# Kernel optimization log

Measured on AMD Instinct MI355X. Metric: run time of the kernel, lower is better.

The kernel has to match this reference:

```python
import math
import jax, jax.numpy as jnp
import numpy as np

B, S, D, H = 2, 2048, 1024, 16
DH = D // H
DFF = 4 * D
EPS = 1e-6
MASKED_BIAS = -10000.0


def _gelu(x):
    # GPT-2 tanh-approx GELU
    return 0.5 * x * (1.0 + jnp.tanh(math.sqrt(2.0 / math.pi) * (x + 0.044715 * x ** 3)))


def _layernorm(x, w, b):
    mean = jnp.mean(x, axis=-1, keepdims=True)
    var = jnp.mean((x - mean) ** 2, axis=-1, keepdims=True)
    return w * ((x - mean) / jnp.sqrt(var + EPS)) + b


def setup_inputs() -> dict:
    key = jax.random.key(0)
    ks = jax.random.split(key, 6)
    std = 0.02
    return {
        "hidden_states": jax.random.normal(ks[0], (B, S, D), jnp.float32),
        "w_attn": jax.random.normal(ks[1], (D, 3 * D), jnp.float32) * std,
        "b_attn": jnp.zeros((3 * D,), jnp.float32),
        "w_proj": jax.random.normal(ks[2], (D, D), jnp.float32) * std,
        "b_proj": jnp.zeros((D,), jnp.float32),
        "w_fc": jax.random.normal(ks[3], (D, DFF), jnp.float32) * std,
        "b_fc": jnp.zeros((DFF,), jnp.float32),
        "w_fc_proj": jax.random.normal(ks[4], (DFF, D), jnp.float32) * std,
        "b_fc_proj": jnp.zeros((D,), jnp.float32),
        "ln1_w": jnp.ones((D,), jnp.float32),
        "ln1_b": jnp.zeros((D,), jnp.float32),
        "ln2_w": jnp.ones((D,), jnp.float32),
        "ln2_b": jnp.zeros((D,), jnp.float32),
    }


def reference(hidden_states, w_attn, b_attn, w_proj, b_proj, w_fc, b_fc,
              w_fc_proj, b_fc_proj, ln1_w, ln1_b, ln2_w, ln2_b):
    residual = hidden_states
    x = _layernorm(hidden_states, ln1_w, ln1_b)

    # c_attn: [B,S,D] @ [D,3D] + b -> split into q,k,v
    qkv = x @ w_attn + b_attn
    q, k, v = jnp.split(qkv, 3, axis=-1)
    # split heads -> [B,H,S,DH]
    q = q.reshape(B, S, H, DH).transpose(0, 2, 1, 3)
    k = k.reshape(B, S, H, DH).transpose(0, 2, 1, 3)
    v = v.reshape(B, S, H, DH).transpose(0, 2, 1, 3)

    scores = jnp.einsum('bhqd,bhkd->bhqk', q, k) / jnp.sqrt(jnp.float32(DH))
    causal = jnp.tril(jnp.ones((S, S), bool))  # [S,S]
    scores = jnp.where(causal[None, None], scores, jnp.float32(MASKED_BIAS))
    attn = jax.nn.softmax(scores, axis=-1)
    out = jnp.einsum('bhqk,bhkd->bhqd', attn, v)
    out = out.transpose(0, 2, 1, 3).reshape(B, S, D)
    out = out @ w_proj + b_proj

    h = residual + out
    residual = h
    y = _layernorm(h, ln2_w, ln2_b)
    y = _gelu(y @ w_fc + b_fc)
    y = y @ w_fc_proj + b_fc_proj
    return residual + y
```

## Files before the change

kernel.cpp:

```cpp
#include <hip/hip_runtime.h>
#include <cstdint>
#include <cstddef>

typedef unsigned short u16;
typedef float  floatx4 __attribute__((ext_vector_type(4)));
typedef short  short8  __attribute__((ext_vector_type(8)));
typedef u16    usx4    __attribute__((ext_vector_type(4)));
typedef u16    usx8    __attribute__((ext_vector_type(8)));
typedef unsigned uintx2 __attribute__((ext_vector_type(2)));

__device__ __forceinline__ u16 f2b(float f) {
  unsigned u = __float_as_uint(f);
  unsigned r = u + 0x7fffu + ((u >> 16) & 1u);
  return (u16)(r >> 16);
}
__device__ __forceinline__ float b2f(u16 s) {
  return __uint_as_float(((unsigned)s) << 16);
}

__device__ __forceinline__ unsigned cvt_pk_bf16(float lo, float hi) {
  unsigned r;
  asm("v_cvt_pk_bf16_f32 %0, %1, %2" : "=v"(r) : "v"(lo), "v"(hi));
  return r;
}

__device__ __forceinline__ float rowmax16(float x) {
  int xi = __float_as_int(x), y;
  y = __builtin_amdgcn_update_dpp(xi, xi, 0xB1, 0xF, 0xF, false);
  x = fmaxf(x, __int_as_float(y)); xi = __float_as_int(x);
  y = __builtin_amdgcn_update_dpp(xi, xi, 0x4E, 0xF, 0xF, false);
  x = fmaxf(x, __int_as_float(y)); xi = __float_as_int(x);
  y = __builtin_amdgcn_update_dpp(xi, xi, 0x141, 0xF, 0xF, false);
  x = fmaxf(x, __int_as_float(y)); xi = __float_as_int(x);
  y = __builtin_amdgcn_update_dpp(xi, xi, 0x140, 0xF, 0xF, false);
  x = fmaxf(x, __int_as_float(y));
  return x;
}

__device__ __forceinline__ float gelu_f(float x) {
  const float k = 2.3022082f;
  float u = x * (1.0f + 0.044715f * x * x);
  float t = __builtin_amdgcn_exp2f(-k * u);
  return x * __builtin_amdgcn_rcpf(1.0f + t);
}

__device__ __forceinline__ void gl2lds16(const u16* g, u16* l) {
  __builtin_amdgcn_global_load_lds(
      (const __attribute__((address_space(1))) unsigned int*)g,
      (__attribute__((address_space(3))) unsigned int*)l, 16, 0, 0);
}

template<int N> __device__ __forceinline__ void wait_stage_barrier() {
  asm volatile("s_waitcnt vmcnt(%0)" :: "n"(N) : "memory");
  __builtin_amdgcn_s_barrier();
  __builtin_amdgcn_sched_barrier(0);
}

#define C2SCALE 0.18033688011112042f

__global__ __launch_bounds__(256) void ln_bf16_kernel(
    const float* __restrict__ in, const float* __restrict__ w,
    const float* __restrict__ b, u16* __restrict__ out)
{
  const int row = blockIdx.x;
  const int t = threadIdx.x;
  const float* p = in + (size_t)row * 1024 + t * 4;
  floatx4 v = *(const floatx4*)p;
  float s  = v.x + v.y + v.z + v.w;
  float ss = v.x*v.x + v.y*v.y + v.z*v.z + v.w*v.w;
  #pragma unroll
  for (int m = 1; m < 64; m <<= 1) {
    s  += __shfl_xor(s,  m);
    ss += __shfl_xor(ss, m);
  }
  __shared__ float red[8];
  if ((t & 63) == 0) { red[(t >> 6)*2] = s; red[(t >> 6)*2 + 1] = ss; }
  __syncthreads();
  s  = red[0] + red[2] + red[4] + red[6];
  ss = red[1] + red[3] + red[5] + red[7];
  const float mean = s * (1.0f / 1024.0f);
  const float var  = ss * (1.0f / 1024.0f) - mean * mean;
  const float rstd = rsqrtf(var + 1e-6f);
  floatx4 wv = *(const floatx4*)(w + t * 4);
  floatx4 bv = *(const floatx4*)(b + t * 4);
  usx4 o = { f2b(wv.x * ((v.x - mean) * rstd) + bv.x),
             f2b(wv.y * ((v.y - mean) * rstd) + bv.y),
             f2b(wv.z * ((v.z - mean) * rstd) + bv.z),
             f2b(wv.w * ((v.w - mean) * rstd) + bv.w) };
  *(usx4*)(out + (size_t)row * 1024 + t * 4) = o;
}

template<int NP>
__global__ __launch_bounds__(256) void combine_ln_kernel(
    const u16* __restrict__ pp, size_t pstride,
    const float* __restrict__ res, const float* __restrict__ bias,
    const float* __restrict__ w, const float* __restrict__ b,
    float* __restrict__ hout, u16* __restrict__ yout)
{
  const int row = blockIdx.x;
  const int t = threadIdx.x;
  const size_t i0 = (size_t)row * 1024 + t * 4;
  floatx4 rv = *(const floatx4*)(res + i0);
  usx4 a[NP];
  #pragma unroll
  for (int z = 0; z < NP; ++z) a[z] = *(const usx4*)(pp + z * pstride + i0);
  floatx4 biasv = *(const floatx4*)(bias + t * 4);
  floatx4 v;
  #pragma unroll
  for (int i = 0; i < 4; ++i) {
    float acc = rv[i] + biasv[i];
    #pragma unroll
    for (int z = 0; z < NP; ++z) acc += b2f(a[z][i]);
    v[i] = acc;
  }
  *(floatx4*)(hout + i0) = v;

  float s  = v.x + v.y + v.z + v.w;
  float ss = v.x*v.x + v.y*v.y + v.z*v.z + v.w*v.w;
  #pragma unroll
  for (int m = 1; m < 64; m <<= 1) {
    s  += __shfl_xor(s,  m);
    ss += __shfl_xor(ss, m);
  }
  __shared__ float red[8];
  if ((t & 63) == 0) { red[(t >> 6)*2] = s; red[(t >> 6)*2 + 1] = ss; }
  __syncthreads();
  s  = red[0] + red[2] + red[4] + red[6];
  ss = red[1] + red[3] + red[5] + red[7];
  const float mean = s * (1.0f / 1024.0f);
  const float var  = ss * (1.0f / 1024.0f) - mean * mean;
  const float rstd = rsqrtf(var + 1e-6f);
  floatx4 wv = *(const floatx4*)(w + t * 4);
  floatx4 bv = *(const floatx4*)(b + t * 4);
  usx4 o = { f2b(wv.x * ((v.x - mean) * rstd) + bv.x),
             f2b(wv.y * ((v.y - mean) * rstd) + bv.y),
             f2b(wv.z * ((v.z - mean) * rstd) + bv.z),
             f2b(wv.w * ((v.w - mean) * rstd) + bv.w) };
  *(usx4*)(yout + i0) = o;
}

__device__ __forceinline__ void wtrans_body(
    const float* __restrict__ in, u16* __restrict__ out, int K, int N,
    int bx, int by, int tx, int ty)
{
  __shared__ u16 tile[32][33];
  const int n0 = bx * 32, k0 = by * 32;
  #pragma unroll
  for (int i = 0; i < 4; ++i)
    tile[ty + i*8][tx] = f2b(in[(size_t)(k0 + ty + i*8) * N + n0 + tx]);
  __syncthreads();
  #pragma unroll
  for (int i = 0; i < 4; ++i)
    out[(size_t)(n0 + ty + i*8) * K + k0 + tx] = tile[tx][ty + i*8];
}

__global__ __launch_bounds__(256) void wtrans4_kernel(
    const float* __restrict__ w0, const float* __restrict__ w1,
    const float* __restrict__ w2, const float* __restrict__ w3,
    u16* __restrict__ o0, u16* __restrict__ o1,
    u16* __restrict__ o2, u16* __restrict__ o3)
{
  int blk = blockIdx.x;
  const int tx = threadIdx.x & 31, ty = threadIdx.x >> 5;
  if (blk < 3072) {
    wtrans_body(w0, o0, 1024, 3072, blk % 96, blk / 96, tx, ty);
  } else if (blk < 4096) {
    blk -= 3072; wtrans_body(w1, o1, 1024, 1024, blk % 32, blk / 32, tx, ty);
  } else if (blk < 8192) {
    blk -= 4096; wtrans_body(w2, o2, 1024, 4096, blk % 128, blk / 128, tx, ty);
  } else {
    blk -= 8192; wtrans_body(w3, o3, 4096, 1024, blk % 32, blk / 32, tx, ty);
  }
}

template<int FLAGS, int NX, int NY, int NZ, int RX, int RY, int RZ>
__global__ __launch_bounds__(512, 2) void gemm256_kernel(
    const u16* __restrict__ A, const u16* __restrict__ Bt,
    const float* __restrict__ bias,
    void* __restrict__ Cout, int M, int N, int K, int kLen, size_t zStride)
{
  constexpr int SLOT = 256 * 32;
  constexpr int GX = NX / RX, GY = NY / RY, GZ = NZ / RZ;
  __shared__ u16 As[2][2][SLOT];
  __shared__ u16 Bs[2][2][SLOT];

  const int lin = blockIdx.x + NX * (blockIdx.y + NY * blockIdx.z);
  const int xcd = lin & 7;
  const int idx = lin >> 3;
  const int rx = xcd % RX, ry = (xcd / RX) % RY, rz = xcd / (RX * RY);
  const int bx = rx * GX + idx % GX;
  const int by = ry * GY + (idx / GX) % GY;
  const int bz = rz * GZ + idx / (GX * GY);

  const int t = threadIdx.x;
  const int wave = t >> 6;
  const int lane = t & 63;
  const int quad = lane >> 4, l16 = lane & 15;
  const int wm = wave >> 2;
  const int wn = wave & 3;
  const int bm0 = by * 256, bn0 = bx * 256;
  const int kStart = bz * kLen;

  const int sRow = lane >> 2;
  const int sq   = (lane & 3) ^ ((lane >> 3) & 3);

  const u16* aGb[2]; const u16* bGb[2];
  #pragma unroll
  for (int j = 0; j < 2; ++j) {
    const int band = wave * 2 + j;
    aGb[j] = A  + (size_t)(bm0 + band * 16 + sRow) * K + kStart + sq * 8;
    bGb[j] = Bt + (size_t)(bn0 + band * 16 + sRow) * K + kStart + sq * 8;
  }

  auto stageA = [&](int kt, int kk) {
    u16* dst = &As[kt & 1][kk][0];
    #pragma unroll
    for (int j = 0; j < 2; ++j)
      gl2lds16(aGb[j] + kt * 64 + kk * 32, dst + (wave * 2 + j) * 512);
  };
  auto stageB = [&](int kt, int kk) {
    u16* dst = &Bs[kt & 1][kk][0];
    #pragma unroll
    for (int j = 0; j < 2; ++j)
      gl2lds16(bGb[j] + kt * 64 + kk * 32, dst + (wave * 2 + j) * 512);
  };

  floatx4 acc[8][4] = {};
  const int rcol = (quad ^ ((l16 >> 1) & 3)) << 3;

  const int NT = kLen >> 6;
  stageA(0, 0); stageB(0, 0); stageA(0, 1); stageB(0, 1);

  #pragma unroll 1
  for (int kt = 0; kt < NT; ++kt) {
    const int buf = kt & 1;
    const bool pf = (kt + 1 < NT);
    short8 af[4], bf[4];

    wait_stage_barrier<4>();
    #pragma unroll
    for (int nt2 = 0; nt2 < 4; ++nt2)
      bf[nt2] = *(const short8*)&Bs[buf][0][(wn*64 + nt2*16 + l16) * 32 + rcol];
    #pragma unroll
    for (int mt = 0; mt < 4; ++mt)
      af[mt] = *(const short8*)&As[buf][0][(wm*128 + mt*16 + l16) * 32 + rcol];
    if (pf) stageA(kt + 1, 0);
    __builtin_amdgcn_s_barrier();
    asm volatile("s_waitcnt lgkmcnt(0)" ::: "memory");
    __builtin_amdgcn_sched_barrier(0);
    __builtin_amdgcn_s_setprio(1);
    #pragma unroll
    for (int mt = 0; mt < 4; ++mt)
      #pragma unroll
      for (int nt2 = 0; nt2 < 4; ++nt2)
        acc[mt][nt2] = __builtin_amdgcn_mfma_f32_16x16x32_bf16(af[mt], bf[nt2], acc[mt][nt2], 0, 0, 0);
    __builtin_amdgcn_s_setprio(0);
    __builtin_amdgcn_s_barrier();
    #pragma unroll
    for (int mt = 0; mt < 4; ++mt)
      af[mt] = *(const short8*)&As[buf][0][(wm*128 + (mt+4)*16 + l16) * 32 + rcol];
    if (pf) stageB(kt + 1, 0);
    __builtin_amdgcn_s_barrier();
    asm volatile("s_waitcnt lgkmcnt(0)" ::: "memory");
    __builtin_amdgcn_sched_barrier(0);
    __builtin_amdgcn_s_setprio(1);
    #pragma unroll
    for (int mt = 0; mt < 4; ++mt)
      #pragma unroll
      for (int nt2 = 0; nt2 < 4; ++nt2)
        acc[mt+4][nt2] = __builtin_amdgcn_mfma_f32_16x16x32_bf16(af[mt], bf[nt2], acc[mt+4][nt2], 0, 0, 0);
    __builtin_amdgcn_s_setprio(0);
    if (pf) wait_stage_barrier<4>(); else wait_stage_barrier<0>();
    #pragma unroll
    for (int nt2 = 0; nt2 < 4; ++nt2)
      bf[nt2] = *(const short8*)&Bs[buf][1][(wn*64 + nt2*16 + l16) * 32 + rcol];
    #pragma unroll
    for (int mt = 0; mt < 4; ++mt)
      af[mt] = *(const short8*)&As[buf][1][(wm*128 + mt*16 + l16) * 32 + rcol];
    if (pf) stageA(kt + 1, 1);
    __builtin_amdgcn_s_barrier();
    asm volatile("s_waitcnt lgkmcnt(0)" ::: "memory");
    __builtin_amdgcn_sched_barrier(0);
    __builtin_amdgcn_s_setprio(1);
    #pragma unroll
    for (int mt = 0; mt < 4; ++mt)
      #pragma unroll
      for (int nt2 = 0; nt2 < 4; ++nt2)
        acc[mt][nt2] = __builtin_amdgcn_mfma_f32_16x16x32_bf16(af[mt], bf[nt2], acc[mt][nt2], 0, 0, 0);
    __builtin_amdgcn_s_setprio(0);
    __builtin_amdgcn_s_barrier();
    #pragma unroll
    for (int mt = 0; mt < 4; ++mt)
      af[mt] = *(const short8*)&As[buf][1][(wm*128 + (mt+4)*16 + l16) * 32 + rcol];
    if (pf) stageB(kt + 1, 1);
    __builtin_amdgcn_s_barrier();
    asm volatile("s_waitcnt lgkmcnt(0)" ::: "memory");
    __builtin_amdgcn_sched_barrier(0);
    __builtin_amdgcn_s_setprio(1);
    #pragma unroll
    for (int mt = 0; mt < 4; ++mt)
      #pragma unroll
      for (int nt2 = 0; nt2 < 4; ++nt2)
        acc[mt+4][nt2] = __builtin_amdgcn_mfma_f32_16x16x32_bf16(af[mt], bf[nt2], acc[mt+4][nt2], 0, 0, 0);
    __builtin_amdgcn_s_setprio(0);
  }

  const int orow0 = bm0 + wm * 128;
  const int ocol0 = bn0 + wn * 64;
  const size_t zoff = (size_t)bz * zStride;
  #pragma unroll
  for (int nt2 = 0; nt2 < 4; ++nt2) {
    const int col = ocol0 + nt2*16 + l16;
    const float bv = bias ? bias[col] : 0.0f;
    const float postscale = ((FLAGS & 8) && col < 1024) ? C2SCALE : 1.0f;
    #pragma unroll
    for (int mt = 0; mt < 8; ++mt) {
      #pragma unroll
      for (int r = 0; r < 4; ++r) {
        const int row = orow0 + mt*16 + quad*4 + r;
        float v = acc[mt][nt2][r] + bv;
        if (FLAGS & 1) v = gelu_f(v);
        if (FLAGS & 8) v *= postscale;
        if (FLAGS & 4) ((u16*)Cout)[zoff + (size_t)row * N + col] = f2b(v);
        else           ((float*)Cout)[zoff + (size_t)row * N + col] = v;
      }
    }
  }
}

__global__ __launch_bounds__(256, 4) void attn_mfma_kernel(
    const u16* __restrict__ qkv, u16* __restrict__ opart, float* __restrict__ ml)
{
  __shared__ u16 Ks[64][72];
  __shared__ u16 Vt[64][72];
  __shared__ u16 Ps[64][72];

  const int t    = threadIdx.x;
  const int wave = t >> 6;
  const int lane = t & 63;
  const int quad = lane >> 4;
  const int l16  = lane & 15;
  const int pair = blockIdx.x >> 1;
  const int half = blockIdx.x & 1;
  const int h    = blockIdx.y;
  const int b    = blockIdx.z;

  const size_t base = (size_t)b * 2048 * 3072;
  const int qoff = h * 64;
  const int koff = 1024 + h * 64;
  const int voff = 2048 + h * 64;

  const int prow = t >> 2;
  const int scol = (t & 3) * 16;
  const int kmap = ((prow & 15) << 2) | (prow >> 4);
  const int kpair  = t & 31;
  const int vchunk = t >> 5;

  const size_t obase  = ((((size_t)half * 2 + b) * 16 + h) * 2048) * 64;
  const size_t mlbase = ((((size_t)half * 2 + b) * 16 + h) * 2048) * 2;

  short8 onesb;
  {
    const short v = (l16 == 0) ? (short)0x3F80 : (short)0;
    #pragma unroll
    for (int i = 0; i < 8; ++i) onesb[i] = v;
  }

  #pragma unroll 1
  for (int iter = 0; iter < 2; ++iter) {
    const int qi = iter ? (31 - pair) : pair;
    const int q0 = qi << 6;
    const int T  = qi + 1;
    const int mid = (T + 1) >> 1;
    const int t0 = half ? mid : 0;
    const int t1 = half ? T : mid;

    floatx4 of[4] = {};
    floatx4 ofl = {};
    float m[4];
    #pragma unroll
    for (int r = 0; r < 4; ++r) m[r] = -1e30f;

    if (t0 < t1) {
      __syncthreads();
      {
        const u16* qp = qkv + base + (size_t)(q0 + prow) * 3072 + qoff + scol;
        *(usx8*)&Ks[prow][scol]     = *(const usx8*)qp;
        *(usx8*)&Ks[prow][scol + 8] = *(const usx8*)(qp + 8);
      }
      __syncthreads();
      const short8 qf0 = *(const short8*)&Ks[wave*16 + l16][quad*8];
      const short8 qf1 = *(const short8*)&Ks[wave*16 + l16][32 + quad*8];

      usx8 kr0, kr1, vr0, vr1;
      {
        const int k0 = t0 << 6;
        const u16* kp = qkv + base + (size_t)(k0 + kmap) * 3072 + koff + scol;
        kr0 = *(const usx8*)kp; kr1 = *(const usx8*)(kp + 8);
        const u16* vp = qkv + base + (size_t)(k0 + 2*kpair) * 3072 + voff + vchunk*8;
        vr0 = *(const usx8*)vp; vr1 = *(const usx8*)(vp + 3072);
      }

      for (int tIdx = t0; tIdx < t1; ++tIdx) {
        __syncthreads();
        *(usx8*)&Ks[prow][scol]     = kr0;
        *(usx8*)&Ks[prow][scol + 8] = kr1;
        #pragma unroll
        for (int i = 0; i < 8; ++i)
          *(unsigned*)&Vt[vchunk*8 + i][2*kpair] =
              (unsigned)vr0[i] | ((unsigned)vr1[i] << 16);
        __syncthreads();

        if (tIdx + 1 < t1) {
          const int kn = (tIdx + 1) << 6;
          const u16* kp = qkv + base + (size_t)(kn + kmap) * 3072 + koff + scol;
          kr0 = *(const usx8*)kp; kr1 = *(const usx8*)(kp + 8);
          const u16* vp = qkv + base + (size_t)(kn + 2*kpair) * 3072 + voff + vchunk*8;
          vr0 = *(const usx8*)vp; vr1 = *(const usx8*)(vp + 3072);
        }

        const int k0 = tIdx << 6;
        floatx4 sf[4];
        #pragma unroll
        for (int kt = 0; kt < 4; ++kt) {
          short8 kf0 = *(const short8*)&Ks[kt*16 + l16][quad*8];
          short8 kf1 = *(const short8*)&Ks[kt*16 + l16][32 + quad*8];
          floatx4 z = {};
          z      = __builtin_amdgcn_mfma_f32_16x16x32_bf16(qf0, kf0, z, 0, 0, 0);
          sf[kt] = __builtin_amdgcn_mfma_f32_16x16x32_bf16(qf1, kf1, z, 0, 0, 0);
        }

        const bool diag = (tIdx == qi);
        #pragma unroll
        for (int r = 0; r < 4; ++r) {
          float sv0 = sf[0][r], sv1 = sf[1][r], sv2 = sf[2][r], sv3 = sf[3][r];
          if (diag) {
            const int qrow = q0 + wave*16 + quad*4 + r;
            const int kbase = k0 + 4*l16;
            if (kbase     > qrow) sv0 = -1e30f;
            if (kbase + 1 > qrow) sv1 = -1e30f;
            if (kbase + 2 > qrow) sv2 = -1e30f;
            if (kbase + 3 > qrow) sv3 = -1e30f;
          }
          float mx = fmaxf(fmaxf(sv0, sv1), fmaxf(sv2, sv3));
          mx = rowmax16(mx);
          const float nm = fmaxf(m[r], mx);
          const float alpha = __builtin_amdgcn_exp2f(m[r] - nm);
          m[r] = nm;
          const float p0 = __builtin_amdgcn_exp2f(sv0 - nm);
          const float p1 = __builtin_amdgcn_exp2f(sv1 - nm);
          const float p2 = __builtin_amdgcn_exp2f(sv2 - nm);
          const float p3 = __builtin_amdgcn_exp2f(sv3 - nm);
          uintx2 pw = { cvt_pk_bf16(p0, p1), cvt_pk_bf16(p2, p3) };
          *(uintx2*)&Ps[wave*16 + quad*4 + r][l16 * 4] = pw;
          #pragma unroll
          for (int dht = 0; dht < 4; ++dht) of[dht][r] *= alpha;
          ofl[r] *= alpha;
        }

        short8 pf0 = *(const short8*)&Ps[wave*16 + l16][quad*8];
        short8 pf1 = *(const short8*)&Ps[wave*16 + l16][32 + quad*8];
        #pragma unroll
        for (int dht = 0; dht < 4; ++dht) {
          short8 vf0 = *(const short8*)&Vt[dht*16 + l16][quad*8];
          short8 vf1 = *(const short8*)&Vt[dht*16 + l16][32 + quad*8];
          of[dht] = __builtin_amdgcn_mfma_f32_16x16x32_bf16(pf0, vf0, of[dht], 0, 0, 0);
          of[dht] = __builtin_amdgcn_mfma_f32_16x16x32_bf16(pf1, vf1, of[dht], 0, 0, 0);
        }
        ofl = __builtin_amdgcn_mfma_f32_16x16x32_bf16(pf0, onesb, ofl, 0, 0, 0);
        ofl = __builtin_amdgcn_mfma_f32_16x16x32_bf16(pf1, onesb, ofl, 0, 0, 0);
      }
    }

    #pragma unroll
    for (int r = 0; r < 4; ++r) {
      const int s = q0 + wave*16 + quad*4 + r;
      u16* orow = opart + obase + (size_t)s * 64;
      #pragma unroll
      for (int dht = 0; dht < 4; ++dht) orow[dht*16 + l16] = f2b(of[dht][r]);
      const float lr = __shfl(ofl[r], quad * 16);
      if (l16 == 0) { ml[mlbase + 2*s] = m[r]; ml[mlbase + 2*s + 1] = lr; }
    }
  }
}

__global__ __launch_bounds__(256) void attn_combine_kernel(
    const u16* __restrict__ opart, const float* __restrict__ ml,
    u16* __restrict__ out)
{
  const int t = threadIdx.x;
  const int s = blockIdx.x * 4 + (t >> 6);
  const int lane = t & 63;
  const int h = blockIdx.y, b = blockIdx.z;

  const size_t o0  = ((((size_t)0 * 2 + b) * 16 + h) * 2048 + s) * 64 + lane;
  const size_t o1  = ((((size_t)1 * 2 + b) * 16 + h) * 2048 + s) * 64 + lane;
  const size_t ml0 = ((((size_t)0 * 2 + b) * 16 + h) * 2048 + s) * 2;
  const size_t ml1 = ((((size_t)1 * 2 + b) * 16 + h) * 2048 + s) * 2;

  const float m0 = ml[ml0], l0 = ml[ml0 + 1];
  const float m1 = ml[ml1], l1 = ml[ml1 + 1];
  const float M  = fmaxf(m0, m1);
  const float w0 = __builtin_amdgcn_exp2f(m0 - M);
  const float w1 = __builtin_amdgcn_exp2f(m1 - M);
  const float L  = w0 * l0 + w1 * l1;
  const float o  = w0 * b2f(opart[o0]) + w1 * b2f(opart[o1]);
  out[((size_t)b * 2048 + s) * 1024 + h * 64 + lane] = f2b(o / L);
}

template<int NP>
__global__ __launch_bounds__(256) void ksplit_combine_kernel(
    const u16* __restrict__ pp, size_t pstride,
    const float* __restrict__ res, const float* __restrict__ bias,
    float* __restrict__ out)
{
  const size_t i0 = ((size_t)blockIdx.x * 256 + threadIdx.x) * 8;
  usx8 a[NP];
  #pragma unroll
  for (int z = 0; z < NP; ++z) a[z] = *(const usx8*)(pp + z * pstride + i0);
  const int col = (int)(i0 & 1023);
  floatx4 bv0 = *(const floatx4*)(bias + col);
  floatx4 bv1 = *(const floatx4*)(bias + col + 4);
  floatx4 h0 = *(const floatx4*)(res + i0);
  floatx4 h1 = *(const floatx4*)(res + i0 + 4);
  floatx4 o0, o1;
  #pragma unroll
  for (int i = 0; i < 4; ++i) {
    float s0 = h0[i] + bv0[i], s1 = h1[i] + bv1[i];
    #pragma unroll
    for (int z = 0; z < NP; ++z) { s0 += b2f(a[z][i]); s1 += b2f(a[z][4+i]); }
    o0[i] = s0; o1[i] = s1;
  }
  *(floatx4*)(out + i0)     = o0;
  *(floatx4*)(out + i0 + 4) = o1;
}

extern "C" void kernel_launch(void* const* d_in, const int* in_sizes, int n_in,
                              void* d_out, int out_size, void* d_ws, size_t ws_size,
                              hipStream_t stream) {
  const float* hidden    = (const float*)d_in[0];
  const float* w_attn    = (const float*)d_in[1];
  const float* b_attn    = (const float*)d_in[2];
  const float* w_proj    = (const float*)d_in[3];
  const float* b_proj    = (const float*)d_in[4];
  const float* w_fc      = (const float*)d_in[5];
  const float* b_fc      = (const float*)d_in[6];
  const float* w_fc_proj = (const float*)d_in[7];
  const float* b_fc_proj = (const float*)d_in[8];
  const float* ln1_w     = (const float*)d_in[9];
  const float* ln1_b     = (const float*)d_in[10];
  const float* ln2_w     = (const float*)d_in[11];
  const float* ln2_b     = (const float*)d_in[12];

  char* wsb = (char*)d_ws;
  u16*   qkvb  = (u16*)  (wsb + (size_t)( 0u << 20));
  u16*   xb    = (u16*)  (wsb + (size_t)(24u << 20));
  u16*   opart = (u16*)  (wsb + (size_t)(24u << 20));
  float* mlbuf = (float*)(wsb + (size_t)(40u << 20));
  u16*   attnb = (u16*)  (wsb + (size_t)(42u << 20));
  u16*   wqT   = (u16*)  (wsb + (size_t)(50u << 20));
  u16*   wpT   = (u16*)  (wsb + (size_t)(56u << 20));
  u16*   wfT   = (u16*)  (wsb + (size_t)(58u << 20));
  u16*   wfpT  = (u16*)  (wsb + (size_t)(66u << 20));
  u16*   pproj = (u16*)  (wsb + (size_t)(24u << 20));
  float* hbuf  = (float*)(wsb + (size_t)(42u << 20));
  u16*   yb    = (u16*)  (wsb + (size_t)( 0u << 20));
  u16*   fcb   = (u16*)  (wsb + (size_t)( 8u << 20));
  u16*   p4    = (u16*)  (wsb + (size_t)(74u << 20));
  u16*   pfcp0 = (u16*)  (wsb + (size_t)( 0u << 20));
  const size_t zstr8  = ((size_t)8u << 20) / 2;
  const size_t zstr58 = ((size_t)58u << 20) / 2;

  const bool big = ws_size >= ((size_t)106u << 20);

  wtrans4_kernel<<<dim3(12288), 256, 0, stream>>>(
      w_attn, w_proj, w_fc, w_fc_proj, wqT, wpT, wfT, wfpT);

  ln_bf16_kernel<<<4096, 256, 0, stream>>>(hidden, ln1_w, ln1_b, xb);
  gemm256_kernel<12, 12,16,1, 2,4,1><<<dim3(12, 16, 1), 512, 0, stream>>>(
      xb, wqT, b_attn, qkvb, 4096, 3072, 1024, 1024, 0);
  attn_mfma_kernel<<<dim3(32, 16, 2), 256, 0, stream>>>(qkvb, opart, mlbuf);
  attn_combine_kernel<<<dim3(512, 16, 2), 256, 0, stream>>>(opart, mlbuf, attnb);

  if (big) {
    gemm256_kernel<4, 4,16,4, 1,2,4><<<dim3(4, 16, 4), 512, 0, stream>>>(
        attnb, wpT, nullptr, p4, 4096, 1024, 1024, 256, zstr8);
    combine_ln_kernel<4><<<4096, 256, 0, stream>>>(
        p4, zstr8, hidden, b_proj, ln2_w, ln2_b, hbuf, yb);
  } else {
    gemm256_kernel<4, 4,16,2, 1,4,2><<<dim3(4, 16, 2), 512, 0, stream>>>(
        attnb, wpT, nullptr, pproj, 4096, 1024, 1024, 512, zstr8);
    combine_ln_kernel<2><<<4096, 256, 0, stream>>>(
        pproj, zstr8, hidden, b_proj, ln2_w, ln2_b, hbuf, yb);
  }
  gemm256_kernel<5, 16,16,1, 2,4,1><<<dim3(16, 16, 1), 512, 0, stream>>>(
      yb, wfT, b_fc, fcb, 4096, 4096, 1024, 1024, 0);
  if (big) {
    gemm256_kernel<4, 4,16,4, 1,2,4><<<dim3(4, 16, 4), 512, 0, stream>>>(
        fcb, wfpT, nullptr, p4, 4096, 1024, 4096, 1024, zstr8);
    ksplit_combine_kernel<4><<<dim3(2048), 256, 0, stream>>>(
        p4, zstr8, hbuf, b_fc_proj, (float*)d_out);
  } else {
    gemm256_kernel<4, 4,16,2, 1,4,2><<<dim3(4, 16, 2), 512, 0, stream>>>(
        fcb, wfpT, nullptr, pfcp0, 4096, 1024, 4096, 2048, zstr58);
    ksplit_combine_kernel<2><<<dim3(2048), 256, 0, stream>>>(
        pfcp0, zstr58, hbuf, b_fc_proj, (float*)d_out);
  }
}
```

Measured before the change: 358.1 us.

## Add 128x128 GEMM kernel for QKV, reorder prefetch, stage epilogue via LDS

Adds a new 256-thread 128x128-tile bf16 MFMA GEMM with double-buffered direct-to-LDS loads and uses it for the QKV projection in place of the 256x256 kernel. The goal is more blocks in flight for better CU occupancy. The 256-tile kernel also issues its next-stage prefetches before its LDS fragment reads. Its epilogue now writes bf16 results through LDS and stores them as coalesced 16-byte rows. The new epilogue always writes bf16, which matches the remaining callers but would break any fp32-output use.

```diff
diff --git a/kernel.cpp b/kernel.cpp
--- a/kernel.cpp
+++ b/kernel.cpp
@@ -52,6 +52,11 @@
 
 template<int N> __device__ __forceinline__ void wait_stage_barrier() {
   asm volatile("s_waitcnt vmcnt(%0)" :: "n"(N) : "memory");
+  __builtin_amdgcn_s_barrier();
+  __builtin_amdgcn_sched_barrier(0);
+}
+__device__ __forceinline__ void post_barrier() {
+  __builtin_amdgcn_sched_barrier(0);
   __builtin_amdgcn_s_barrier();
   __builtin_amdgcn_sched_barrier(0);
 }
@@ -173,6 +178,127 @@
   }
 }
 
+template<int BM, int BN, int FLAGS, int MINW,
+         int NX, int NY, int NZ, int RX, int RY, int RZ>
+__global__ __launch_bounds__(256, MINW) void gemm_mfma_kernel(
+    const u16* __restrict__ A, const u16* __restrict__ Bt,
+    const float* __restrict__ bias, const float* __restrict__ Res,
+    void* __restrict__ Cout, int M, int N, int K, int kLen, size_t zStride)
+{
+  constexpr int WM = BM / 2, WN = BN / 2;
+  constexpr int MT = WM / 16, NT = WN / 16;
+  constexpr int GX = NX / RX, GY = NY / RY, GZ = NZ / RZ;
+  constexpr int ABUF = BM * 32, BBUF = BN * 32;
+  constexpr int L = BM / 64 + BN / 64;
+  __shared__ u16 As[2 * ABUF];
+  __shared__ u16 Bs[2 * BBUF];
+
+  const int lin = blockIdx.x + NX * (blockIdx.y + NY * blockIdx.z);
+  const int xcd = lin & 7;
+  const int idx = lin >> 3;
+  const int rx = xcd % RX, ry = (xcd / RX) % RY, rz = xcd / (RX * RY);
+  const int bx = rx * GX + idx % GX;
+  const int by = ry * GY + (idx / GX) % GY;
+  const int bz = rz * GZ + idx / (GX * GY);
+
+  const int t = threadIdx.x;
+  const int wave = t >> 6, lane = t & 63;
+  const int quad = lane >> 4, l16 = lane & 15;
+  const int wm = wave >> 1, wn = wave & 1;
+  const int bm0 = by * BM, bn0 = bx * BN;
+  const int kStart = bz * kLen;
+
+  const int sRow = lane >> 2;
+  const int sq   = (lane & 3) ^ ((lane >> 4) & 3);
+
+  const u16* aG[BM / 64];
+  u16* aL[BM / 64];
+  #pragma unroll
+  for (int j = 0; j < BM / 64; ++j) {
+    const int band = j * 4 + wave;
+    aG[j] = A + (size_t)(bm0 + band * 16 + sRow) * K + kStart + sq * 8;
+    aL[j] = As + band * 512;
+  }
+  const u16* bG[BN / 64];
+  u16* bL[BN / 64];
+  #pragma unroll
+  for (int j = 0; j < BN / 64; ++j) {
+    const int band = j * 4 + wave;
+    bG[j] = Bt + (size_t)(bn0 + band * 16 + sRow) * K + kStart + sq * 8;
+    bL[j] = Bs + band * 512;
+  }
+
+  floatx4 acc[MT][NT] = {};
+  const int rcol = (quad ^ (l16 >> 2)) << 3;
+
+  auto stage = [&](int tile, int buf) {
+    #pragma unroll
+    for (int j = 0; j < BM / 64; ++j) gl2lds16(aG[j] + tile * 32, aL[j] + buf * ABUF);
+    #pragma unroll
+    for (int j = 0; j < BN / 64; ++j) gl2lds16(bG[j] + tile * 32, bL[j] + buf * BBUF);
+  };
+  auto compute = [&](int buf) {
+    const u16* Asc = As + buf * ABUF;
+    const u16* Bsc = Bs + buf * BBUF;
+    short8 af[MT], bf[NT];
+    #pragma unroll
+    for (int mt = 0; mt < MT; ++mt)
+      af[mt] = *(const short8*)&Asc[(wm*WM + mt*16 + l16) * 32 + rcol];
+    #pragma unroll
+    for (int nt = 0; nt < NT; ++nt)
+      bf[nt] = *(const short8*)&Bsc[(wn*WN + nt*16 + l16) * 32 + rcol];
+    __builtin_amdgcn_s_setprio(1);
+    #pragma unroll
+    for (int mt = 0; mt < MT; ++mt)
+      #pragma unroll
+      for (int nt = 0; nt < NT; ++nt)
+        acc[mt][nt] = __builtin_amdgcn_mfma_f32_16x16x32_bf16(af[mt], bf[nt], acc[mt][nt], 0, 0, 0);
+    __builtin_amdgcn_s_setprio(0);
+  };
+
+  const int nt = kLen >> 5;
+  stage(0, 0);
+  stage(1, 1);
+  #pragma unroll 1
+  for (int ti = 0; ti < nt - 2; ti += 2) {
+    wait_stage_barrier<L>();
+    compute(0);
+    post_barrier();
+    stage(ti + 2, 0);
+    wait_stage_barrier<L>();
+    compute(1);
+    post_barrier();
+    stage(ti + 3, 1);
+  }
+  wait_stage_barrier<L>();
+  compute(0);
+  wait_stage_barrier<0>();
+  compute(1);
+
+  const int orow0 = bm0 + wm * WM;
+  const int ocol0 = bn0 + wn * WN;
+  const size_t zoff = (size_t)bz * zStride;
+  #pragma unroll
+  for (int nt2 = 0; nt2 < NT; ++nt2) {
+    const int col = ocol0 + nt2*16 + l16;
+    const float bv = bias ? bias[col] : 0.0f;
+    const float postscale = ((FLAGS & 8) && col < 1024) ? C2SCALE : 1.0f;
+    #pragma unroll
+    for (int mt = 0; mt < MT; ++mt) {
+      #pragma unroll
+      for (int r = 0; r < 4; ++r) {
+        const int row = orow0 + mt*16 + quad*4 + r;
+        float v = acc[mt][nt2][r] + bv;
+        if (FLAGS & 1) v = gelu_f(v);
+        if (FLAGS & 8) v *= postscale;
+        if (FLAGS & 2) v += Res[(size_t)row * N + col];
+        if (FLAGS & 4) ((u16*)Cout)[zoff + (size_t)row * N + col] = f2b(v);
+        else           ((float*)Cout)[zoff + (size_t)row * N + col] = v;
+      }
+    }
+  }
+}
+
 template<int FLAGS, int NX, int NY, int NZ, int RX, int RY, int RZ>
 __global__ __launch_bounds__(512, 2) void gemm256_kernel(
     const u16* __restrict__ A, const u16* __restrict__ Bt,
@@ -238,13 +364,13 @@
     short8 af[4], bf[4];
 
     wait_stage_barrier<4>();
+    if (pf) stageA(kt + 1, 0);
     #pragma unroll
     for (int nt2 = 0; nt2 < 4; ++nt2)
       bf[nt2] = *(const short8*)&Bs[buf][0][(wn*64 + nt2*16 + l16) * 32 + rcol];
     #pragma unroll
     for (int mt = 0; mt < 4; ++mt)
       af[mt] = *(const short8*)&As[buf][0][(wm*128 + mt*16 + l16) * 32 + rcol];
-    if (pf) stageA(kt + 1, 0);
     __builtin_amdgcn_s_barrier();
     asm volatile("s_waitcnt lgkmcnt(0)" ::: "memory");
     __builtin_amdgcn_sched_barrier(0);
@@ -256,10 +382,10 @@
         acc[mt][nt2] = __builtin_amdgcn_mfma_f32_16x16x32_bf16(af[mt], bf[nt2], acc[mt][nt2], 0, 0, 0);
     __builtin_amdgcn_s_setprio(0);
     __builtin_amdgcn_s_barrier();
+    if (pf) stageB(kt + 1, 0);
     #pragma unroll
     for (int mt = 0; mt < 4; ++mt)
       af[mt] = *(const short8*)&As[buf][0][(wm*128 + (mt+4)*16 + l16) * 32 + rcol];
-    if (pf) stageB(kt + 1, 0);
     __builtin_amdgcn_s_barrier();
     asm volatile("s_waitcnt lgkmcnt(0)" ::: "memory");
     __builtin_amdgcn_sched_barrier(0);
@@ -271,13 +397,13 @@
         acc[mt+4][nt2] = __builtin_amdgcn_mfma_f32_16x16x32_bf16(af[mt], bf[nt2], acc[mt+4][nt2], 0, 0, 0);
     __builtin_amdgcn_s_setprio(0);
     if (pf) wait_stage_barrier<4>(); else wait_stage_barrier<0>();
+    if (pf) stageA(kt + 1, 1);
     #pragma unroll
     for (int nt2 = 0; nt2 < 4; ++nt2)
       bf[nt2] = *(const short8*)&Bs[buf][1][(wn*64 + nt2*16 + l16) * 32 + rcol];
     #pragma unroll
     for (int mt = 0; mt < 4; ++mt)
       af[mt] = *(const short8*)&As[buf][1][(wm*128 + mt*16 + l16) * 32 + rcol];
-    if (pf) stageA(kt + 1, 1);
     __builtin_amdgcn_s_barrier();
     asm volatile("s_waitcnt lgkmcnt(0)" ::: "memory");
     __builtin_amdgcn_sched_barrier(0);
@@ -289,10 +415,10 @@
         acc[mt][nt2] = __builtin_amdgcn_mfma_f32_16x16x32_bf16(af[mt], bf[nt2], acc[mt][nt2], 0, 0, 0);
     __builtin_amdgcn_s_setprio(0);
     __builtin_amdgcn_s_barrier();
+    if (pf) stageB(kt + 1, 1);
     #pragma unroll
     for (int mt = 0; mt < 4; ++mt)
       af[mt] = *(const short8*)&As[buf][1][(wm*128 + (mt+4)*16 + l16) * 32 + rcol];
-    if (pf) stageB(kt + 1, 1);
     __builtin_amdgcn_s_barrier();
     asm volatile("s_waitcnt lgkmcnt(0)" ::: "memory");
     __builtin_amdgcn_sched_barrier(0);
@@ -308,22 +434,33 @@
   const int orow0 = bm0 + wm * 128;
   const int ocol0 = bn0 + wn * 64;
   const size_t zoff = (size_t)bz * zStride;
+  u16* eb = &As[0][0][0] + wave * 1056;
+
+  float bvv[4]; float psv[4];
   #pragma unroll
   for (int nt2 = 0; nt2 < 4; ++nt2) {
     const int col = ocol0 + nt2*16 + l16;
-    const float bv = bias ? bias[col] : 0.0f;
-    const float postscale = ((FLAGS & 8) && col < 1024) ? C2SCALE : 1.0f;
-    #pragma unroll
-    for (int mt = 0; mt < 8; ++mt) {
+    bvv[nt2] = bias ? bias[col] : 0.0f;
+    psv[nt2] = ((FLAGS & 8) && col < 1024) ? C2SCALE : 1.0f;
+  }
+  #pragma unroll 1
+  for (int mt = 0; mt < 8; ++mt) {
+    #pragma unroll
+    for (int nt2 = 0; nt2 < 4; ++nt2) {
       #pragma unroll
       for (int r = 0; r < 4; ++r) {
-        const int row = orow0 + mt*16 + quad*4 + r;
-        float v = acc[mt][nt2][r] + bv;
+        float v = acc[mt][nt2][r] + bvv[nt2];
         if (FLAGS & 1) v = gelu_f(v);
-        if (FLAGS & 8) v *= postscale;
-        if (FLAGS & 4) ((u16*)Cout)[zoff + (size_t)row * N + col] = f2b(v);
-        else           ((float*)Cout)[zoff + (size_t)row * N + col] = v;
+        if (FLAGS & 8) v *= psv[nt2];
+        eb[(quad*4 + r) * 66 + nt2*16 + l16] = f2b(v);
       }
+    }
+    #pragma unroll
+    for (int half = 0; half < 2; ++half) {
+      const int row = half*8 + (lane >> 3);
+      const int co  = (lane & 7) * 8;
+      usx8 val = *(const usx8*)&eb[row * 66 + co];
+      *(usx8*)((u16*)Cout + zoff + (size_t)(orow0 + mt*16 + row) * N + ocol0 + co) = val;
     }
   }
 }
@@ -577,8 +714,8 @@
       w_attn, w_proj, w_fc, w_fc_proj, wqT, wpT, wfT, wfpT);
 
   ln_bf16_kernel<<<4096, 256, 0, stream>>>(hidden, ln1_w, ln1_b, xb);
-  gemm256_kernel<12, 12,16,1, 2,4,1><<<dim3(12, 16, 1), 512, 0, stream>>>(
-      xb, wqT, b_attn, qkvb, 4096, 3072, 1024, 1024, 0);
+  gemm_mfma_kernel<128,128,12,4, 24,32,1, 2,4,1><<<dim3(24, 32, 1), 256, 0, stream>>>(
+      xb, wqT, b_attn, nullptr, qkvb, 4096, 3072, 1024, 1024, 0);
   attn_mfma_kernel<<<dim3(32, 16, 2), 256, 0, stream>>>(qkvb, opart, mlbuf);
   attn_combine_kernel<<<dim3(512, 16, 2), 256, 0, stream>>>(opart, mlbuf, attnb);
 
```

After: 428.0 us. 19.5% more time.
